# Performance work log

Measured on AMD Instinct MI355X. Metric: run time of the kernel, lower is better.

Reference implementation:

```python
import jax, jax.numpy as jnp
import numpy as np

FEATURES_DIM = 100000
NUM_FIELDS = 39
EMBED_DIM = 64
DIM_INT = (2, 3)
RANK = (32, 32)
BATCH = 8192


def setup_inputs() -> dict:
    key = jax.random.key(0)
    ks = jax.random.split(key, 6)
    x = jax.random.randint(ks[0], (BATCH, NUM_FIELDS), 0, FEATURES_DIM)
    embed_table = jax.random.normal(ks[1], (FEATURES_DIM, EMBED_DIM), dtype=jnp.float32) * 0.01
    linear_w = jax.random.normal(ks[2], (FEATURES_DIM, 1), dtype=jnp.float32) * 0.01
    linear_bias = jnp.zeros((1,), dtype=jnp.float32)
    # trunc_normal_(std=0.01) approximated by clipped normal
    W0 = jnp.clip(jax.random.normal(ks[3], (DIM_INT[0], RANK[0], NUM_FIELDS), dtype=jnp.float32) * 0.01, -0.02, 0.02)
    W1 = jnp.clip(jax.random.normal(ks[4], (DIM_INT[1], RANK[1], NUM_FIELDS), dtype=jnp.float32) * 0.01, -0.02, 0.02)
    return {"x": x, "embed_table": embed_table, "linear_w": linear_w,
            "linear_bias": linear_bias, "W0": W0, "W1": W1}


def _calc_cross(W, emb):
    # W: (l, j, k) = (dim_int, rank, num_fields); emb: (b, k, i) = (batch, fields, embed)
    # dot_products[b,i,j,l] = sum_k W[l,j,k] * emb[b,k,i]
    dp = jnp.einsum('ljk,bki->bijl', W, emb)          # (b, embed, rank, dim_int)
    prod_over_l = jnp.prod(dp, axis=3)                # (b, embed, rank)
    return jnp.sum(prod_over_l, axis=(1, 2))          # (b,)


def reference(x, embed_table, linear_w, linear_bias, W0, W1):
    emb = embed_table[x]                              # (b, fields, embed)
    lin = jnp.sum(linear_w[x], axis=1) + linear_bias  # (b, 1)
    ret = lin[:, 0] + _calc_cross(W0, emb) + _calc_cross(W1, emb)
    return ret                                        # (b,)
```

## Files before the change

### kernel.cpp

```cpp
#include <hip/hip_runtime.h>

#define BATCH    8192
#define NF       39
#define ED       64
#define RANK     32
#define NFRAG    15

typedef _Float16 half8  __attribute__((ext_vector_type(8)));
typedef float    f32x16 __attribute__((ext_vector_type(16)));

__global__ void prep_w(const float* __restrict__ W0,
                       const float* __restrict__ W1,
                       half8* __restrict__ wsW) {
    int d = blockIdx.x * 256 + threadIdx.x;
    if (d >= NFRAG * 64) return;
    int fid  = d >> 6;
    int lane = d & 63;
    int l = fid / 3, kc = fid % 3;
    int j = lane & 31, kh = lane >> 5;
    const float* base = (l < 2) ? (W0 + (l * RANK + j) * NF)
                                : (W1 + ((l - 2) * RANK + j) * NF);
    half8 h;
#pragma unroll
    for (int e = 0; e < 8; ++e) {
        int k = kc * 16 + kh * 8 + e;
        h[e] = (k < NF) ? (_Float16)base[k] : (_Float16)0.0f;
    }
    wsW[d] = h;
}

union H8U { half8 h; unsigned int u[4]; };

__device__ __forceinline__ void glds16(const void* g, void* l) {
    __builtin_amdgcn_global_load_lds(
        (const __attribute__((address_space(1))) unsigned int*)g,
        (__attribute__((address_space(3))) unsigned int*)l, 16, 0, 0);
}

__global__ __launch_bounds__(256, 3) void tfm_kernel(
    const int*   __restrict__ x,
    const float* __restrict__ embed,
    const float* __restrict__ linw,
    const float* __restrict__ lbias,
    const half8* __restrict__ wsW,
    float*       __restrict__ out)
{
    __shared__ __align__(16) _Float16 Ws[NFRAG * 64 * 8];

    const int t    = threadIdx.x;
    const int lane = t & 63;
    const int w    = t >> 6;
    const int s    = blockIdx.x * 4 + w;

    const int srow = __builtin_amdgcn_readfirstlane(s);
    const int* __restrict__ xrow = x + srow * NF;
    int xi[NF];
#pragma unroll
    for (int k = 0; k < NF; ++k) xi[k] = xrow[k];

    const int xi_v = (lane < NF) ? x[s * NF + lane] : 0;

    float r[NF];
#pragma unroll
    for (int k = 0; k < NF; ++k)
        r[k] = embed[(size_t)xi[k] * ED + lane];

#pragma unroll
    for (int i = 0; i < 4; ++i) {
        int c = w + i * 4;
        if (c < NFRAG)
            glds16(&wsW[c * 64 + lane], &Ws[(c * 64 + lane) * 8]);
    }

    const float lv   = (lane < NF) ? linw[xi_v] : 0.0f;
    const float bias = lbias[0];

    half8 bf0[3], bf1[3];
#pragma unroll
    for (int kc = 0; kc < 3; ++kc) {
        H8U A, B;
#pragma unroll
        for (int e = 0; e < 8; ++e) {
            int kA = kc * 16 + e;
            int kB = kc * 16 + 8 + e;
            A.h[e] = (kA < NF) ? (_Float16)r[kA] : (_Float16)0.0f;
            B.h[e] = (kB < NF) ? (_Float16)r[kB] : (_Float16)0.0f;
        }
#pragma unroll
        for (int q = 0; q < 4; ++q)
            asm volatile("v_permlane32_swap_b32 %0, %1"
                         : "+v"(A.u[q]), "+v"(B.u[q]));
        bf0[kc] = A.h;
        bf1[kc] = B.h;
    }

    __syncthreads();

    const half8* Wf = (const half8*)Ws;
    float ssum = lv;

    f32x16 z;
#pragma unroll
    for (int e = 0; e < 16; ++e) z[e] = 0.0f;

#define TILE_BODY(BF)                                                          \
    {                                                                          \
        f32x16 a0 = __builtin_amdgcn_mfma_f32_32x32x16_f16(                    \
                        Wf[(0 * 3 + 0) * 64 + lane], BF[0], z, 0, 0, 0);       \
        f32x16 a1 = __builtin_amdgcn_mfma_f32_32x32x16_f16(                    \
                        Wf[(1 * 3 + 0) * 64 + lane], BF[0], z, 0, 0, 0);       \
        _Pragma("unroll")                                                      \
        for (int kc = 1; kc < 3; ++kc) {                                       \
            a0 = __builtin_amdgcn_mfma_f32_32x32x16_f16(                       \
                     Wf[(0 * 3 + kc) * 64 + lane], BF[kc], a0, 0, 0, 0);       \
            a1 = __builtin_amdgcn_mfma_f32_32x32x16_f16(                       \
                     Wf[(1 * 3 + kc) * 64 + lane], BF[kc], a1, 0, 0, 0);       \
        }                                                                      \
        float p0 = 0.f, p1 = 0.f, p2 = 0.f, p3 = 0.f;                          \
        _Pragma("unroll")                                                      \
        for (int e = 0; e < 4; ++e) {                                          \
            p0 += a0[e]      * a1[e];                                          \
            p1 += a0[4 + e]  * a1[4 + e];                                      \
            p2 += a0[8 + e]  * a1[8 + e];                                      \
            p3 += a0[12 + e] * a1[12 + e];                                     \
        }                                                                      \
        ssum += (p0 + p1) + (p2 + p3);                                         \
        f32x16 c0 = __builtin_amdgcn_mfma_f32_32x32x16_f16(                    \
                        Wf[(2 * 3 + 0) * 64 + lane], BF[0], z, 0, 0, 0);       \
        f32x16 c1 = __builtin_amdgcn_mfma_f32_32x32x16_f16(                    \
                        Wf[(3 * 3 + 0) * 64 + lane], BF[0], z, 0, 0, 0);       \
        f32x16 c2 = __builtin_amdgcn_mfma_f32_32x32x16_f16(                    \
                        Wf[(4 * 3 + 0) * 64 + lane], BF[0], z, 0, 0, 0);       \
        _Pragma("unroll")                                                      \
        for (int kc = 1; kc < 3; ++kc) {                                       \
            c0 = __builtin_amdgcn_mfma_f32_32x32x16_f16(                       \
                     Wf[(2 * 3 + kc) * 64 + lane], BF[kc], c0, 0, 0, 0);       \
            c1 = __builtin_amdgcn_mfma_f32_32x32x16_f16(                       \
                     Wf[(3 * 3 + kc) * 64 + lane], BF[kc], c1, 0, 0, 0);       \
            c2 = __builtin_amdgcn_mfma_f32_32x32x16_f16(                       \
                     Wf[(4 * 3 + kc) * 64 + lane], BF[kc], c2, 0, 0, 0);       \
        }                                                                      \
        float q0 = 0.f, q1 = 0.f, q2 = 0.f, q3 = 0.f;                          \
        _Pragma("unroll")                                                      \
        for (int e = 0; e < 4; ++e) {                                          \
            q0 += c0[e]      * c1[e]      * c2[e];                             \
            q1 += c0[4 + e]  * c1[4 + e]  * c2[4 + e];                         \
            q2 += c0[8 + e]  * c1[8 + e]  * c2[8 + e];                         \
            q3 += c0[12 + e] * c1[12 + e] * c2[12 + e];                        \
        }                                                                      \
        ssum += (q0 + q1) + (q2 + q3);                                         \
    }

    TILE_BODY(bf0)
    TILE_BODY(bf1)
#undef TILE_BODY

#pragma unroll
    for (int off = 32; off > 0; off >>= 1) ssum += __shfl_down(ssum, off, 64);
    if (lane == 0) out[s] = ssum + bias;
}

extern "C" void kernel_launch(void* const* d_in, const int* in_sizes, int n_in,
                              void* d_out, int out_size, void* d_ws, size_t ws_size,
                              hipStream_t stream) {
    const int*   x     = (const int*)  d_in[0];
    const float* embed = (const float*)d_in[1];
    const float* linw  = (const float*)d_in[2];
    const float* lbias = (const float*)d_in[3];
    const float* W0    = (const float*)d_in[4];
    const float* W1    = (const float*)d_in[5];
    float*       out   = (float*)d_out;
    half8*       wsW   = (half8*)d_ws;

    prep_w<<<(NFRAG * 64 + 255) / 256, 256, 0, stream>>>(W0, W1, wsW);
    tfm_kernel<<<BATCH / 4, 256, 0, stream>>>(x, embed, linw, lbias, wsW, out);
}
```

Before: 93.51 us.

## Pre-convert embedding table to fp16 and gather half-width rows

Adds a prep pass that converts the full embedding table to fp16 in workspace, fused with the existing weight fragment packing. The main kernel then gathers fp16 rows, halving the bytes per random gather. In exchange each call pays a full streaming read and write of the table, which may outweigh the gather savings if the gathers were cache-bound.

```diff
diff --git a/kernel.cpp b/kernel.cpp
--- a/kernel.cpp
+++ b/kernel.cpp
@@ -5,28 +5,41 @@
 #define ED       64
 #define RANK     32
 #define NFRAG    15
+#define TBL      100000
 
 typedef _Float16 half8  __attribute__((ext_vector_type(8)));
+typedef _Float16 half4v __attribute__((ext_vector_type(4)));
 typedef float    f32x16 __attribute__((ext_vector_type(16)));
 
-__global__ void prep_w(const float* __restrict__ W0,
-                       const float* __restrict__ W1,
-                       half8* __restrict__ wsW) {
-    int d = blockIdx.x * 256 + threadIdx.x;
-    if (d >= NFRAG * 64) return;
-    int fid  = d >> 6;
-    int lane = d & 63;
-    int l = fid / 3, kc = fid % 3;
-    int j = lane & 31, kh = lane >> 5;
-    const float* base = (l < 2) ? (W0 + (l * RANK + j) * NF)
-                                : (W1 + ((l - 2) * RANK + j) * NF);
-    half8 h;
+__global__ __launch_bounds__(256) void prep(
+        const float* __restrict__ embed,
+        const float* __restrict__ W0,
+        const float* __restrict__ W1,
+        _Float16*    __restrict__ embf16,
+        half8*       __restrict__ wsW) {
+    int i = blockIdx.x * 256 + threadIdx.x;
+    {
+        float4 v = ((const float4*)embed)[i];
+        half4v h;
+        h[0] = (_Float16)v.x; h[1] = (_Float16)v.y;
+        h[2] = (_Float16)v.z; h[3] = (_Float16)v.w;
+        ((half4v*)embf16)[i] = h;
+    }
+    if (i < NFRAG * 64) {
+        int fid  = i >> 6;
+        int lane = i & 63;
+        int l = fid / 3, kc = fid % 3;
+        int j = lane & 31, kh = lane >> 5;
+        const float* base = (l < 2) ? (W0 + (l * RANK + j) * NF)
+                                    : (W1 + ((l - 2) * RANK + j) * NF);
+        half8 h;
 #pragma unroll
-    for (int e = 0; e < 8; ++e) {
-        int k = kc * 16 + kh * 8 + e;
-        h[e] = (k < NF) ? (_Float16)base[k] : (_Float16)0.0f;
+        for (int e = 0; e < 8; ++e) {
+            int k = kc * 16 + kh * 8 + e;
+            h[e] = (k < NF) ? (_Float16)base[k] : (_Float16)0.0f;
+        }
+        wsW[i] = h;
     }
-    wsW[d] = h;
 }
 
 union H8U { half8 h; unsigned int u[4]; };
@@ -38,12 +51,12 @@
 }
 
 __global__ __launch_bounds__(256, 3) void tfm_kernel(
-    const int*   __restrict__ x,
-    const float* __restrict__ embed,
-    const float* __restrict__ linw,
-    const float* __restrict__ lbias,
-    const half8* __restrict__ wsW,
-    float*       __restrict__ out)
+    const int*      __restrict__ x,
+    const _Float16* __restrict__ embf16,
+    const float*    __restrict__ linw,
+    const float*    __restrict__ lbias,
+    const half8*    __restrict__ wsW,
+    float*          __restrict__ out)
 {
     __shared__ __align__(16) _Float16 Ws[NFRAG * 64 * 8];
 
@@ -60,10 +73,10 @@
 
     const int xi_v = (lane < NF) ? x[s * NF + lane] : 0;
 
-    float r[NF];
+    _Float16 rh[NF];
 #pragma unroll
     for (int k = 0; k < NF; ++k)
-        r[k] = embed[(size_t)xi[k] * ED + lane];
+        rh[k] = embf16[(size_t)xi[k] * ED + lane];
 
 #pragma unroll
     for (int i = 0; i < 4; ++i) {
@@ -83,8 +96,8 @@
         for (int e = 0; e < 8; ++e) {
             int kA = kc * 16 + e;
             int kB = kc * 16 + 8 + e;
-            A.h[e] = (kA < NF) ? (_Float16)r[kA] : (_Float16)0.0f;
-            B.h[e] = (kB < NF) ? (_Float16)r[kB] : (_Float16)0.0f;
+            A.h[e] = (kA < NF) ? rh[kA] : (_Float16)0.0f;
+            B.h[e] = (kB < NF) ? rh[kB] : (_Float16)0.0f;
         }
 #pragma unroll
         for (int q = 0; q < 4; ++q)
@@ -170,8 +183,10 @@
     const float* W0    = (const float*)d_in[4];
     const float* W1    = (const float*)d_in[5];
     float*       out   = (float*)d_out;
-    half8*       wsW   = (half8*)d_ws;
 
-    prep_w<<<(NFRAG * 64 + 255) / 256, 256, 0, stream>>>(W0, W1, wsW);
-    tfm_kernel<<<BATCH / 4, 256, 0, stream>>>(x, embed, linw, lbias, wsW, out);
+    _Float16* embf16 = (_Float16*)d_ws;
+    half8*    wsW    = (half8*)((char*)d_ws + (size_t)13 * 1024 * 1024);
+
+    prep<<<(TBL * ED / 4 + 255) / 256, 256, 0, stream>>>(embed, W0, W1, embf16, wsW);
+    tfm_kernel<<<BATCH / 4, 256, 0, stream>>>(x, embf16, linw, lbias, wsW, out);
 }
```

Measured after the change: 94.75 us. No clear change (+1.3%).
